# Optimization experiments

Hardware: AMD Instinct MI355X
Metric: run time of the kernel (lower is better)

Reference implementation:

```python
import jax, jax.numpy as jnp
import numpy as np

L, N, H = 131072, 256, 256
R_MIN, R_MAX, MAX_PHASE = 0.0, 1.0, 6.28


def _binop(ei, ej):
    a_i, bu_i = ei
    a_j, bu_j = ej
    return a_j * a_i, a_j * bu_i + bu_j


def setup_inputs() -> dict:
    key = jax.random.key(0)
    kx, k1, k2, kbr, kbi, kcr, kci, kd = jax.random.split(key, 8)
    u1 = jax.random.uniform(k1, (N,))
    u2 = jax.random.uniform(k2, (N,))
    nu_log = jnp.log(-0.5 * jnp.log(u1 * (R_MAX**2 - R_MIN**2) + R_MIN**2))
    theta_log = jnp.log(MAX_PHASE * u2)
    B_re = jax.random.normal(kbr, (N, H)) / jnp.sqrt(2.0 * H)
    B_im = jax.random.normal(kbi, (N, H)) / jnp.sqrt(2.0 * H)
    C_re = jax.random.normal(kcr, (H, N)) / jnp.sqrt(1.0 * N)
    C_im = jax.random.normal(kci, (H, N)) / jnp.sqrt(1.0 * N)
    D = jax.random.normal(kd, (H,))
    diag_lambda = jnp.exp(-jnp.exp(nu_log) + 1j * jnp.exp(theta_log))
    gamma_log = jnp.log(jnp.sqrt(1.0 - jnp.abs(diag_lambda) ** 2))
    x = jax.random.normal(kx, (L, H), dtype=jnp.float32)
    return {"x": x, "nu_log": nu_log, "theta_log": theta_log,
            "B_re": B_re, "B_im": B_im, "C_re": C_re, "C_im": C_im,
            "D": D, "gamma_log": gamma_log}


def reference(x, nu_log, theta_log, B_re, B_im, C_re, C_im, D, gamma_log):
    # Lambda: (N,) complex diagonal recurrence coefficients
    Lambda = jnp.exp(-jnp.exp(nu_log) + 1j * jnp.exp(theta_log))
    B_norm = (B_re + 1j * B_im) * jnp.exp(gamma_log)[:, None]  # (N, H)
    C = C_re + 1j * C_im                                        # (H, N)
    # Input projection: Bu[l] = B_norm @ x[l]  -> (L, N) complex
    Bu = jnp.einsum('nh,lh->ln', B_norm, x.astype(B_norm.dtype))
    Lam = jnp.broadcast_to(Lambda[None, :], Bu.shape)
    # Diagonal linear recurrence z[l] = Lambda * z[l-1] + Bu[l] via associative scan
    _, states = jax.lax.associative_scan(_binop, (Lam, Bu))     # (L, N)
    # Output projection: y = Re(C @ z) + D * u
    y = jnp.einsum('hn,ln->lh', C, states).real + D * x
    return y
```

## Files before the change

### kernel.cpp

```cpp
#include <hip/hip_runtime.h>
#include <math.h>

#define L_SEQ 131072
#define NSTATE 256
#define HDIM   256
#define KDIM   512
#define LC     128
#define NCHUNK (L_SEQ / LC)

typedef __bf16 bf16x8 __attribute__((ext_vector_type(8)));
typedef float  f32x4  __attribute__((ext_vector_type(4)));

__device__ __forceinline__ float bf2f(unsigned short u) {
    unsigned int v = (unsigned int)u << 16;
    float f; __builtin_memcpy(&f, &v, 4); return f;
}
__device__ __forceinline__ unsigned short f2bf(float f) {
    unsigned int v; __builtin_memcpy(&v, &f, 4);
    unsigned int lsb = (v >> 16) & 1u;
    v += 0x7fffu + lsb;
    return (unsigned short)(v >> 16);
}

__device__ __forceinline__ void gl_lds16(const void* g, void* l) {
    __builtin_amdgcn_global_load_lds(
        (const __attribute__((address_space(1))) void*)g,
        (__attribute__((address_space(3))) void*)l, 16, 0, 0);
}

__global__ void prep_kernel(const float* __restrict__ nu_log,
                            const float* __restrict__ theta_log,
                            const float* __restrict__ B_re,
                            const float* __restrict__ B_im,
                            const float* __restrict__ C_re,
                            const float* __restrict__ C_im,
                            const float* __restrict__ gamma_log,
                            unsigned short* __restrict__ W1,
                            unsigned short* __restrict__ W2,
                            float2* __restrict__ Lambda,
                            float2* __restrict__ lamLc) {
    const int bid = blockIdx.x;
    const int tid = threadIdx.x;
    {
        int n = bid, h = tid;
        float g = expf(gamma_log[n]);
        W1[(size_t)(2 * n + 0) * HDIM + h] = f2bf(B_re[(size_t)n * HDIM + h] * g);
        W1[(size_t)(2 * n + 1) * HDIM + h] = f2bf(B_im[(size_t)n * HDIM + h] * g);
    }
    {
        int h = bid, n = tid;
        W2[(size_t)h * KDIM + 2 * n + 0] = f2bf(C_re[(size_t)h * NSTATE + n]);
        W2[(size_t)h * KDIM + 2 * n + 1] = f2bf(-C_im[(size_t)h * NSTATE + n]);
    }
    if (bid == 0) {
        int n = tid;
        float a = expf(nu_log[n]);
        float b = expf(theta_log[n]);
        float r = expf(-a);
        Lambda[n] = make_float2(r * cosf(b), r * sinf(b));
        float rl = expf(-a * (float)LC);
        float bl = b * (float)LC;
        lamLc[n] = make_float2(rl * cosf(bl), rl * sinf(bl));
    }
}

__launch_bounds__(256)
__global__ void castx_kernel(const float* __restrict__ x,
                             unsigned short* __restrict__ xb) {
    size_t i = ((size_t)blockIdx.x * 256 + threadIdx.x) * 8;
    float4 a = *(const float4*)(x + i);
    float4 b = *(const float4*)(x + i + 4);
    union { unsigned short s[8]; uint4 v; } u;
    u.s[0] = f2bf(a.x); u.s[1] = f2bf(a.y); u.s[2] = f2bf(a.z); u.s[3] = f2bf(a.w);
    u.s[4] = f2bf(b.x); u.s[5] = f2bf(b.y); u.s[6] = f2bf(b.z); u.s[7] = f2bf(b.w);
    *(uint4*)(xb + i) = u.v;
}

template <int K, int NT, bool EPI2>
__launch_bounds__(512)
__global__ void gemm_mfma(const unsigned short* __restrict__ A,
                          const unsigned short* __restrict__ B,
                          int ldc,
                          unsigned short* __restrict__ Cb,
                          float* __restrict__ Cf,
                          const float* __restrict__ Dv,
                          const float* __restrict__ x) {
    __shared__ __align__(16) unsigned short lds[4 * 4096];

    const int tid  = threadIdx.x;
    const int wave = tid >> 6;
    const int lane = tid & 63;
    const int quad = lane >> 4;
    const int l16  = lane & 15;
    const int wm   = wave >> 2;
    const int wn   = wave & 3;
    const int srow = lane >> 2;
    const int scol = (lane & 3) * 8;

    const int wg  = blockIdx.y * NT + blockIdx.x;
    const int cpx = (NT * (L_SEQ / 128)) >> 3;
    const int sw  = (wg & 7) * cpx + (wg >> 3);
    const int m0  = (sw / NT) * 128;
    const int n0  = (sw % NT) * 128;

    f32x4 acc[4][2] = {};

    for (int kt = 0; kt < K; kt += 64) {
        {
            const int rr = wave * 16;
            const unsigned short* ga = A + (size_t)(m0 + rr + srow) * K + kt + scol;
            const unsigned short* gb = B + (size_t)(n0 + rr + srow) * K + kt + scol;
            gl_lds16(ga,      lds         + rr * 32);
            gl_lds16(ga + 32, lds + 4096  + rr * 32);
            gl_lds16(gb,      lds + 8192  + rr * 32);
            gl_lds16(gb + 32, lds + 12288 + rr * 32);
        }
        __syncthreads();

        #pragma unroll
        for (int s = 0; s < 2; ++s) {
            const unsigned short* as = lds + s * 4096;
            const unsigned short* bs = lds + 8192 + s * 4096;

            bf16x8 af[4], bfr[2];
            #pragma unroll
            for (int i = 0; i < 4; ++i)
                af[i] = *(const bf16x8*)(as + ((size_t)(wm * 64 + i * 16 + l16)) * 32 + quad * 8);
            #pragma unroll
            for (int j = 0; j < 2; ++j)
                bfr[j] = *(const bf16x8*)(bs + ((size_t)(wn * 32 + j * 16 + l16)) * 32 + quad * 8);
            #pragma unroll
            for (int i = 0; i < 4; ++i)
                #pragma unroll
                for (int j = 0; j < 2; ++j)
                    acc[i][j] = __builtin_amdgcn_mfma_f32_16x16x32_bf16(af[i], bfr[j], acc[i][j], 0, 0, 0);
        }
        __syncthreads();
    }

    #pragma unroll
    for (int i = 0; i < 4; ++i) {
        const int rowb = m0 + wm * 64 + i * 16 + quad * 4;
        #pragma unroll
        for (int j = 0; j < 2; ++j) {
            const int col = n0 + wn * 32 + j * 16 + l16;
            #pragma unroll
            for (int r = 0; r < 4; ++r) {
                const size_t idx = (size_t)(rowb + r) * ldc + col;
                if (EPI2) {
                    Cf[idx] = fmaf(Dv[col], x[idx], acc[i][j][r]);
                } else {
                    Cb[idx] = f2bf(acc[i][j][r]);
                }
            }
        }
    }
}

__launch_bounds__(256)
__global__ void scan1_kernel(const unsigned short* __restrict__ Bu,
                             const float2* __restrict__ Lambda,
                             float2* __restrict__ chunk_local) {
    const int c = blockIdx.x;
    const int n = threadIdx.x;
    const float2 lam = Lambda[n];
    float zr = 0.f, zi = 0.f;
    const unsigned short* p = Bu + (size_t)c * LC * KDIM + 2 * n;
    #pragma unroll 8
    for (int l = 0; l < LC; ++l) {
        unsigned int v = *(const unsigned int*)(p + (size_t)l * KDIM);
        float br = bf2f((unsigned short)(v & 0xffffu));
        float bi = bf2f((unsigned short)(v >> 16));
        float nzr = fmaf(lam.x, zr, fmaf(-lam.y, zi, br));
        float nzi = fmaf(lam.x, zi, fmaf(lam.y, zr, bi));
        zr = nzr; zi = nzi;
    }
    chunk_local[c * NSTATE + n] = make_float2(zr, zi);
}

__launch_bounds__(1024)
__global__ void scan2_kernel(const float2* __restrict__ chunk_local,
                             const float2* __restrict__ lamLc,
                             float2* __restrict__ chunk_prefix) {
    __shared__ float2 sbuf[NCHUNK];
    const int n = blockIdx.x;
    const int c = threadIdx.x;
    float2 lam = lamLc[n];
    float2 b = chunk_local[c * NSTATE + n];
    sbuf[c] = b;
    __syncthreads();
    #pragma unroll
    for (int step = 1; step < NCHUNK; step <<= 1) {
        float2 prev = make_float2(0.f, 0.f);
        if (c >= step) prev = sbuf[c - step];
        __syncthreads();
        if (c >= step) {
            b.x = fmaf(lam.x, prev.x, fmaf(-lam.y, prev.y, b.x));
            b.y = fmaf(lam.x, prev.y, fmaf(lam.y, prev.x, b.y));
        }
        sbuf[c] = b;
        float lr = fmaf(lam.x, lam.x, -lam.y * lam.y);
        float li = 2.f * lam.x * lam.y;
        lam = make_float2(lr, li);
        __syncthreads();
    }
    chunk_prefix[c * NSTATE + n] = b;
}

__launch_bounds__(256)
__global__ void scan3_kernel(unsigned short* __restrict__ Bu,
                             const float2* __restrict__ Lambda,
                             const float2* __restrict__ chunk_prefix) {
    const int c = blockIdx.x;
    const int n = threadIdx.x;
    const float2 lam = Lambda[n];
    float zr = 0.f, zi = 0.f;
    if (c > 0) {
        float2 z0 = chunk_prefix[(c - 1) * NSTATE + n];
        zr = z0.x; zi = z0.y;
    }
    unsigned short* p = Bu + (size_t)c * LC * KDIM + 2 * n;
    #pragma unroll 8
    for (int l = 0; l < LC; ++l) {
        unsigned int v = *(const unsigned int*)(p + (size_t)l * KDIM);
        float br = bf2f((unsigned short)(v & 0xffffu));
        float bi = bf2f((unsigned short)(v >> 16));
        float nzr = fmaf(lam.x, zr, fmaf(-lam.y, zi, br));
        float nzi = fmaf(lam.x, zi, fmaf(lam.y, zr, bi));
        zr = nzr; zi = nzi;
        unsigned int o = (unsigned int)f2bf(nzr) | ((unsigned int)f2bf(nzi) << 16);
        *(unsigned int*)(p + (size_t)l * KDIM) = o;
    }
}

extern "C" void kernel_launch(void* const* d_in, const int* in_sizes, int n_in,
                              void* d_out, int out_size, void* d_ws, size_t ws_size,
                              hipStream_t stream) {
    const float* x         = (const float*)d_in[0];
    const float* nu_log    = (const float*)d_in[1];
    const float* theta_log = (const float*)d_in[2];
    const float* B_re      = (const float*)d_in[3];
    const float* B_im      = (const float*)d_in[4];
    const float* C_re      = (const float*)d_in[5];
    const float* C_im      = (const float*)d_in[6];
    const float* Dvec      = (const float*)d_in[7];
    const float* gamma_log = (const float*)d_in[8];
    float* out = (float*)d_out;

    char* ws = (char*)d_ws;
    const size_t BU_BYTES    = (size_t)L_SEQ * KDIM * 2;
    const size_t XB_BYTES    = (size_t)L_SEQ * HDIM * 2;
    const size_t W1_BYTES    = (size_t)KDIM * HDIM * 2;
    const size_t W2_BYTES    = (size_t)HDIM * KDIM * 2;
    const size_t LAM_BYTES   = (size_t)NSTATE * sizeof(float2);
    const size_t CHUNK_BYTES = (size_t)NCHUNK * NSTATE * sizeof(float2);

    size_t off = 0;
    unsigned short* Bu  = (unsigned short*)(ws + off); off += BU_BYTES;
    unsigned short* xb  = (unsigned short*)(ws + off); off += XB_BYTES;
    unsigned short* W1  = (unsigned short*)(ws + off); off += W1_BYTES;
    unsigned short* W2  = (unsigned short*)(ws + off); off += W2_BYTES;
    float2* Lambda      = (float2*)(ws + off); off += LAM_BYTES;
    float2* lamLc       = (float2*)(ws + off); off += LAM_BYTES;
    float2* chunk_local = (float2*)(ws + off); off += CHUNK_BYTES;
    float2* chunk_pref  = (float2*)(ws + off); off += CHUNK_BYTES;
    if (ws_size < off) return;

    prep_kernel<<<dim3(256), dim3(256), 0, stream>>>(
        nu_log, theta_log, B_re, B_im, C_re, C_im, gamma_log, W1, W2, Lambda, lamLc);

    castx_kernel<<<dim3((L_SEQ * HDIM) / (256 * 8)), dim3(256), 0, stream>>>(x, xb);

    gemm_mfma<HDIM, KDIM / 128, false>
        <<<dim3(KDIM / 128, L_SEQ / 128), dim3(512), 0, stream>>>(
        xb, W1, KDIM, Bu, nullptr, nullptr, nullptr);

    scan1_kernel<<<dim3(NCHUNK), dim3(NSTATE), 0, stream>>>(Bu, Lambda, chunk_local);
    scan2_kernel<<<dim3(NSTATE), dim3(NCHUNK), 0, stream>>>(chunk_local, lamLc, chunk_pref);
    scan3_kernel<<<dim3(NCHUNK), dim3(NSTATE), 0, stream>>>(Bu, Lambda, chunk_pref);

    gemm_mfma<KDIM, HDIM / 128, true>
        <<<dim3(HDIM / 128, L_SEQ / 128), dim3(512), 0, stream>>>(
        Bu, W2, HDIM, nullptr, out, Dvec, x);
}
```

Measured before the change: 458.6 us.

## Triple-buffer LDS K-tiles with async prefetch in MFMA GEMM

Replaces the load-sync-compute-sync loop over 64-wide K tiles with a three-stage ring of 32-wide K tiles. Each tile is prefetched two steps ahead using direct global-to-LDS loads, with explicit vmcnt waits and a single barrier per step. The aim is to overlap global memory latency with MFMA work and cut the barriers per iteration from two to one. In exchange LDS use grows by half, which may lower occupancy, and each step now carries less MFMA work to hide the remaining sync.

```diff
diff --git a/kernel.cpp b/kernel.cpp
--- a/kernel.cpp
+++ b/kernel.cpp
@@ -85,7 +85,7 @@
                           float* __restrict__ Cf,
                           const float* __restrict__ Dv,
                           const float* __restrict__ x) {
-    __shared__ __align__(16) unsigned short lds[4 * 4096];
+    __shared__ __align__(16) unsigned short lds[6 * 4096];
 
     const int tid  = threadIdx.x;
     const int wave = tid >> 6;
@@ -105,37 +105,51 @@
 
     f32x4 acc[4][2] = {};
 
-    for (int kt = 0; kt < K; kt += 64) {
-        {
-            const int rr = wave * 16;
-            const unsigned short* ga = A + (size_t)(m0 + rr + srow) * K + kt + scol;
-            const unsigned short* gb = B + (size_t)(n0 + rr + srow) * K + kt + scol;
-            gl_lds16(ga,      lds         + rr * 32);
-            gl_lds16(ga + 32, lds + 4096  + rr * 32);
-            gl_lds16(gb,      lds + 8192  + rr * 32);
-            gl_lds16(gb + 32, lds + 12288 + rr * 32);
-        }
-        __syncthreads();
-
-        #pragma unroll
-        for (int s = 0; s < 2; ++s) {
-            const unsigned short* as = lds + s * 4096;
-            const unsigned short* bs = lds + 8192 + s * 4096;
-
-            bf16x8 af[4], bfr[2];
-            #pragma unroll
-            for (int i = 0; i < 4; ++i)
-                af[i] = *(const bf16x8*)(as + ((size_t)(wm * 64 + i * 16 + l16)) * 32 + quad * 8);
+    constexpr int T = K / 32;
+
+    auto stage = [&](int t) {
+        const int buf = t % 3;
+        const int rr  = wave * 16;
+        const unsigned short* ga = A + (size_t)(m0 + rr + srow) * K + t * 32 + scol;
+        const unsigned short* gb = B + (size_t)(n0 + rr + srow) * K + t * 32 + scol;
+        gl_lds16(ga, lds + buf * 4096 + rr * 32);
+        gl_lds16(gb, lds + 12288 + buf * 4096 + rr * 32);
+    };
+
+    stage(0);
+    stage(1);
+    asm volatile("s_waitcnt vmcnt(2)" ::: "memory");
+    __builtin_amdgcn_sched_barrier(0);
+    __builtin_amdgcn_s_barrier();
+    __builtin_amdgcn_sched_barrier(0);
+
+    #pragma unroll
+    for (int t = 0; t < T; ++t) {
+        if (t + 2 < T) stage(t + 2);
+
+        const unsigned short* as = lds + (t % 3) * 4096;
+        const unsigned short* bs = lds + 12288 + (t % 3) * 4096;
+
+        bf16x8 af[4], bfr[2];
+        #pragma unroll
+        for (int i = 0; i < 4; ++i)
+            af[i] = *(const bf16x8*)(as + ((size_t)(wm * 64 + i * 16 + l16)) * 32 + quad * 8);
+        #pragma unroll
+        for (int j = 0; j < 2; ++j)
+            bfr[j] = *(const bf16x8*)(bs + ((size_t)(wn * 32 + j * 16 + l16)) * 32 + quad * 8);
+        #pragma unroll
+        for (int i = 0; i < 4; ++i)
             #pragma unroll
             for (int j = 0; j < 2; ++j)
-                bfr[j] = *(const bf16x8*)(bs + ((size_t)(wn * 32 + j * 16 + l16)) * 32 + quad * 8);
-            #pragma unroll
-            for (int i = 0; i < 4; ++i)
-                #pragma unroll
-                for (int j = 0; j < 2; ++j)
-                    acc[i][j] = __builtin_amdgcn_mfma_f32_16x16x32_bf16(af[i], bfr[j], acc[i][j], 0, 0, 0);
+                acc[i][j] = __builtin_amdgcn_mfma_f32_16x16x32_bf16(af[i], bfr[j], acc[i][j], 0, 0, 0);
+
+        if (t + 1 < T) {
+            if (t + 2 < T) { asm volatile("s_waitcnt vmcnt(2)" ::: "memory"); }
+            else           { asm volatile("s_waitcnt vmcnt(0)" ::: "memory"); }
+            __builtin_amdgcn_sched_barrier(0);
+            __builtin_amdgcn_s_barrier();
+            __builtin_amdgcn_sched_barrier(0);
         }
-        __syncthreads();
     }
 
     #pragma unroll
```

Result: no change. 451.4 us (-1.6%).
